# Kernel tuning notes

Hardware: AMD Instinct MI355X
Metric: run time of the kernel (lower is better)

## Reference

```python
import jax, jax.numpy as jnp
import numpy as np

B, T, H, V = 32, 64, 512, 32000


def setup_inputs() -> dict:
    key = jax.random.key(0)
    ks = jax.random.split(key, 8)
    s = 1.0 / np.sqrt(H)
    return {
        "encoder_outputs": jax.random.normal(ks[0], (B, H), dtype=jnp.float32),
        "captions": jax.random.randint(ks[1], (B, T), 0, V),
        "emb": jax.random.normal(ks[2], (V, H), dtype=jnp.float32) * 0.02,
        "W_ih": jax.random.normal(ks[3], (4 * H, 2 * H), dtype=jnp.float32) * s,
        "W_hh": jax.random.normal(ks[4], (4 * H, H), dtype=jnp.float32) * s,
        "b_ih": jnp.zeros((4 * H,), dtype=jnp.float32),
        "b_hh": jnp.zeros((4 * H,), dtype=jnp.float32),
        "W_out": jax.random.normal(ks[5], (V, H), dtype=jnp.float32) * s,
        "b_out": jnp.zeros((V,), dtype=jnp.float32),
    }


def reference(encoder_outputs, captions, emb, W_ih, W_hh, b_ih, b_hh, W_out, b_out):
    Bn, Tn = captions.shape
    Hn = encoder_outputs.shape[-1]
    embeddings = emb[captions]  # (B, T, H)
    # per-step LSTM input: concat(image feature, token embedding) -> (T-1, B, 2H)
    enc = jnp.broadcast_to(encoder_outputs[None], (Tn - 1, Bn, Hn))
    xs = jnp.concatenate([enc, jnp.swapaxes(embeddings[:, : Tn - 1], 0, 1)], axis=-1)
    # precompute input-to-hidden gate contribution outside the scan
    gx = jnp.einsum("tbi,gi->tbg", xs, W_ih) + b_ih  # (T-1, B, 4H)

    h0 = jnp.zeros((Bn, Hn), dtype=encoder_outputs.dtype)
    c0 = jnp.zeros((Bn, Hn), dtype=encoder_outputs.dtype)

    def step(carry, gx_t):
        h, c = carry
        gates = gx_t + h @ W_hh.T + b_hh  # (B, 4H); PyTorch gate order i,f,g,o
        i, f, g, o = jnp.split(gates, 4, axis=-1)
        c = jax.nn.sigmoid(f) * c + jax.nn.sigmoid(i) * jnp.tanh(g)
        h = jax.nn.sigmoid(o) * jnp.tanh(c)
        logit = h @ W_out.T + b_out  # (B, V)
        return (h, c), logit

    _, logits = jax.lax.scan(step, (h0, c0), gx)  # (T-1, B, V)
    logits = jnp.swapaxes(logits, 0, 1)  # (B, T-1, V)
    caption_probs = jnp.max(logits, axis=-1)
    pred_captions = jnp.argmax(logits, axis=-1)
    return logits, caption_probs, pred_captions
```

## Files before the change

kernel.cpp:

```cpp
#include <hip/hip_runtime.h>
#include <hip/hip_bf16.h>
#include <cstdio>


typedef _Float16 half8_t __attribute__((ext_vector_type(8)));
typedef float f32x4_t __attribute__((ext_vector_type(4)));
typedef _Float16 half2_t __attribute__((ext_vector_type(2)));

#define H 512
#define BATCH 32
#define TSTEPS 63
#define G4 2048
#define V 32000

__global__ void k_gxe(const float* __restrict__ enc, const float* __restrict__ W_ih,
                      const float* __restrict__ b_ih, const float* __restrict__ b_hh,
                      float* __restrict__ gxe) {
  __shared__ float sW[16 * 512];
  __shared__ float sP[16 * 8 * 32];
  int tid = threadIdx.x;
  int jg = blockIdx.x;
  #pragma unroll
  for (int rep = 0; rep < 8; ++rep) {
    int q = tid + rep * 256;
    int row = q >> 7, c4 = q & 127;
    float4 v = *(const float4*)(W_ih + (size_t)(jg * 16 + row) * 1024 + c4 * 4);
    *(float4*)(sW + row * 512 + c4 * 4) = v;
  }
  int b = tid & 31, kg = tid >> 5;
  float hreg[64];
  const float* ep = enc + b * 512 + kg * 64;
  #pragma unroll
  for (int i = 0; i < 64; ++i) hreg[i] = ep[i];
  __syncthreads();
  #pragma unroll
  for (int r = 0; r < 16; ++r) {
    float acc = 0.f;
    const float* wp = sW + r * 512 + kg * 64;
    #pragma unroll
    for (int i = 0; i < 64; ++i) acc += hreg[i] * wp[i];
    sP[(r * 8 + kg) * 32 + b] = acc;
  }
  __syncthreads();
  for (int o = tid; o < 512; o += 256) {
    int r = o >> 5, bb = o & 31;
    float s = 0.f;
    #pragma unroll
    for (int k2 = 0; k2 < 8; ++k2) s += sP[(r * 8 + k2) * 32 + bb];
    int j = jg * 16 + r;
    gxe[bb * 2048 + j] = s + b_ih[j] + b_hh[j];
  }
}

__global__ void k_f32_to_f16(const float* __restrict__ src, _Float16* __restrict__ dst) {
  size_t i = ((size_t)blockIdx.x * 256 + threadIdx.x) * 8;
  float4 a = *(const float4*)(src + i);
  float4 b = *(const float4*)(src + i + 4);
  half8_t o;
  o[0] = (_Float16)a.x; o[1] = (_Float16)a.y; o[2] = (_Float16)a.z; o[3] = (_Float16)a.w;
  o[4] = (_Float16)b.x; o[5] = (_Float16)b.y; o[6] = (_Float16)b.z; o[7] = (_Float16)b.w;
  *(half8_t*)(dst + i) = o;
}

__global__ void k_gin(const float* __restrict__ emb, const int* __restrict__ caps,
                      const float* __restrict__ W_ih, const float* __restrict__ gxe,
                      float* __restrict__ ginT) {
  __shared__ float sA[64 * 36];
  __shared__ float sB[64 * 36];
  int tid = threadIdx.x;
  int nb = blockIdx.x;
  int mb = blockIdx.y;
  float acc[4][4] = {};
  int tx = tid & 15, ty = tid >> 4;
  for (int k0 = 0; k0 < 512; k0 += 32) {
    __syncthreads();
    #pragma unroll
    for (int rep = 0; rep < 2; ++rep) {
      int q = tid + rep * 256;
      int row = q >> 3, c4 = q & 7;
      int m = mb * 64 + row;
      int t = m >> 5, b = m & 31;
      if (t > 62) t = 62;
      int tok = caps[b * 64 + t];
      float4 v = *(const float4*)(emb + (size_t)tok * 512 + k0 + c4 * 4);
      *(float4*)(sA + row * 36 + c4 * 4) = v;
      int n = nb * 64 + row;
      float4 w = *(const float4*)(W_ih + (size_t)n * 1024 + 512 + k0 + c4 * 4);
      *(float4*)(sB + row * 36 + c4 * 4) = w;
    }
    __syncthreads();
    #pragma unroll
    for (int kk = 0; kk < 32; ++kk) {
      float a4[4], b4[4];
      #pragma unroll
      for (int i = 0; i < 4; ++i) a4[i] = sA[(ty * 4 + i) * 36 + kk];
      #pragma unroll
      for (int j = 0; j < 4; ++j) b4[j] = sB[(tx * 4 + j) * 36 + kk];
      #pragma unroll
      for (int i = 0; i < 4; ++i)
        #pragma unroll
        for (int j = 0; j < 4; ++j) acc[i][j] += a4[i] * b4[j];
    }
  }
  #pragma unroll
  for (int i = 0; i < 4; ++i) {
    int m = mb * 64 + ty * 4 + i;
    if (m >= 2016) break;
    int t = m >> 5, b = m & 31;
    #pragma unroll
    for (int j = 0; j < 4; ++j) {
      int n = nb * 64 + tx * 4 + j;
      ginT[(size_t)t * 65536 + (size_t)n * 32 + b] = acc[i][j] + gxe[b * 2048 + n];
    }
  }
}

__global__ void k_step(const float* __restrict__ hT_prev, const float* __restrict__ W_hh,
                       const float* __restrict__ ginT_t, float* __restrict__ cT,
                       float* __restrict__ hT_out, _Float16* __restrict__ hf16_t) {
  __shared__ float sW[8 * 512];
  __shared__ float sP[8 * 8 * 32];
  __shared__ float sG[8 * 32];
  int tid = threadIdx.x, kb = blockIdx.x;
  int kbase = kb * 2;
  #pragma unroll
  for (int rep = 0; rep < 4; ++rep) {
    int q = tid + rep * 256;
    int row = q >> 7, c4 = q & 127;
    int j = (row >> 1) * 512 + kbase + (row & 1);
    float4 v = *(const float4*)(W_hh + (size_t)j * 512 + c4 * 4);
    *(float4*)(sW + row * 512 + c4 * 4) = v;
  }
  int b = tid & 31, kg = tid >> 5;
  float hreg[64];
  const float* hp = hT_prev + kg * 64 * 32 + b;
  #pragma unroll
  for (int i = 0; i < 64; ++i) hreg[i] = hp[i * 32];
  __syncthreads();
  #pragma unroll
  for (int r = 0; r < 8; ++r) {
    float acc = 0.f;
    const float* wp = sW + r * 512 + kg * 64;
    #pragma unroll
    for (int i = 0; i < 64; ++i) acc += hreg[i] * wp[i];
    sP[(r * 8 + kg) * 32 + b] = acc;
  }
  __syncthreads();
  {
    int r = tid >> 5;
    float s = 0.f;
    #pragma unroll
    for (int k2 = 0; k2 < 8; ++k2) s += sP[(r * 8 + k2) * 32 + b];
    int j = (r >> 1) * 512 + kbase + (r & 1);
    sG[r * 32 + b] = s + ginT_t[(size_t)j * 32 + b];
  }
  __syncthreads();
  if (tid < 64) {
    int kl = tid >> 5;
    int k = kbase + kl;
    float gi = sG[(0 * 2 + kl) * 32 + b];
    float gf = sG[(1 * 2 + kl) * 32 + b];
    float gg = sG[(2 * 2 + kl) * 32 + b];
    float go = sG[(3 * 2 + kl) * 32 + b];
    float si = 1.f / (1.f + expf(-gi));
    float sf = 1.f / (1.f + expf(-gf));
    float so = 1.f / (1.f + expf(-go));
    float tg = tanhf(gg);
    float c = sf * cT[k * 32 + b] + si * tg;
    float h = so * tanhf(c);
    cT[k * 32 + b] = c;
    hT_out[k * 32 + b] = h;
    hf16_t[(size_t)b * 512 + k] = (_Float16)h;
  }
}

#define ALD 40
__global__ void k_logits(const _Float16* __restrict__ A,
                         const _Float16* __restrict__ B,
                         const float* __restrict__ bias,
                         float* __restrict__ out,
                         float* __restrict__ tmv) {
  __shared__ _Float16 sA[128 * ALD];
  __shared__ _Float16 sB[128 * ALD];
  __shared__ float redv[128 * 2];
  int tid = threadIdx.x;
  int nb = blockIdx.x;
  int mb = blockIdx.y;
  int lane = tid & 63, wave = tid >> 6;
  int wm = wave >> 1, wn = wave & 1;
  const int m0 = mb * 128, n0 = nb * 128;
  f32x4_t acc[4][4] = {};
  int rA = lane & 15, q8 = lane >> 4;
  for (int k0 = 0; k0 < 512; k0 += 32) {
    __syncthreads();
    #pragma unroll
    for (int rep = 0; rep < 2; ++rep) {
      int q = tid + rep * 256;
      int row = q >> 2, seg = q & 3;
      *(half8_t*)(sA + row * ALD + seg * 8) =
          *(const half8_t*)(A + (size_t)(m0 + row) * 512 + k0 + seg * 8);
      *(half8_t*)(sB + row * ALD + seg * 8) =
          *(const half8_t*)(B + (size_t)(n0 + row) * 512 + k0 + seg * 8);
    }
    __syncthreads();
    half8_t afr[4], bfr[4];
    #pragma unroll
    for (int i = 0; i < 4; ++i) {
      afr[i] = *(const half8_t*)(sA + (wm * 64 + i * 16 + rA) * ALD + q8 * 8);
      bfr[i] = *(const half8_t*)(sB + (wn * 64 + i * 16 + rA) * ALD + q8 * 8);
    }
    #pragma unroll
    for (int i = 0; i < 4; ++i)
      #pragma unroll
      for (int j = 0; j < 4; ++j)
        acc[i][j] = __builtin_amdgcn_mfma_f32_16x16x32_f16(afr[i], bfr[j], acc[i][j], 0, 0, 0);
  }
  #pragma unroll
  for (int i = 0; i < 4; ++i) {
    #pragma unroll
    for (int p = 0; p < 4; ++p) {
      int m_loc = wm * 64 + i * 16 + q8 * 4 + p;
      int m = m0 + m_loc;
      float vmax = -3.4e38f;
      float vs[4];
      #pragma unroll
      for (int j = 0; j < 4; ++j) {
        int n_loc = wn * 64 + j * 16 + rA;
        float v = acc[i][j][p] + bias[n0 + n_loc];
        vs[j] = v;
        vmax = fmaxf(vmax, v);
      }
      if (m < 2016) {
        int t = m >> 5, bb = m & 31;
        float* orow = out + (size_t)(bb * 63 + t) * 32000 + n0;
        #pragma unroll
        for (int j = 0; j < 4; ++j) orow[wn * 64 + j * 16 + rA] = vs[j];
      }
      #pragma unroll
      for (int o = 1; o < 16; o <<= 1) vmax = fmaxf(vmax, __shfl_xor(vmax, o));
      if (rA == 0) redv[m_loc * 2 + wn] = vmax;
    }
  }
  __syncthreads();
  if (tid < 128) {
    int m = m0 + tid;
    if (m < 2016) {
      float bv = fmaxf(redv[tid * 2], redv[tid * 2 + 1]);
      tmv[(size_t)m * 256 + nb] = bv;
    }
  }
}

__global__ void k_final(const float* __restrict__ tmv, const float* __restrict__ HallT,
                        const float* __restrict__ Wout, const float* __restrict__ bias,
                        const float* __restrict__ logits,
                        float* __restrict__ probs, float* __restrict__ preds) {
  int m = blockIdx.x;
  int t = m >> 5, b = m & 31;
  int lane = threadIdx.x;
  float mx = -3.4e38f;
  for (int nb = lane; nb < 250; nb += 64) mx = fmaxf(mx, tmv[(size_t)m * 256 + nb]);
  #pragma unroll
  for (int o = 1; o < 64; o <<= 1) mx = fmaxf(mx, __shfl_xor(mx, o));
  const float* hrow = HallT + (size_t)t * 16384 + b;
  float hl[8];
  float s2 = 0.f;
  #pragma unroll
  for (int i = 0; i < 8; ++i) {
    float hv = hrow[(lane * 8 + i) * 32];
    hl[i] = hv;
    s2 += hv * hv;
  }
  #pragma unroll
  for (int o = 1; o < 64; o <<= 1) s2 += __shfl_xor(s2, o);
  float marg = 0.0016f * sqrtf(s2) + 3e-4f;
  float thr = mx - 2.f * marg;
  float bestv = -3.4e38f;
  int besti = 0x7fffffff;
  const float* lrow = logits + (size_t)(b * 63 + t) * 32000;
  for (int nb = 0; nb < 250; ++nb) {
    if (tmv[(size_t)m * 256 + nb] < thr) continue;
    #pragma unroll
    for (int rep = 0; rep < 2; ++rep) {
      int n = nb * 128 + rep * 64 + lane;
      float av = lrow[n];
      unsigned long long mask = __ballot(av >= thr);
      while (mask) {
        int ln = __ffsll((unsigned long long)mask) - 1;
        mask &= mask - 1;
        int nn = __shfl(n, ln);
        const float* wr = Wout + (size_t)nn * 512;
        float p = 0.f;
        #pragma unroll
        for (int i = 0; i < 8; ++i) p += hl[i] * wr[lane * 8 + i];
        #pragma unroll
        for (int o = 1; o < 64; o <<= 1) p += __shfl_xor(p, o);
        p += bias[nn];
        if (p > bestv || (p == bestv && nn < besti)) { bestv = p; besti = nn; }
      }
    }
  }
  if (lane == 0) {
    probs[b * 63 + t] = bestv;
    preds[b * 63 + t] = (float)besti;
  }
}

extern "C" void kernel_launch(void* const* d_in, const int* in_sizes, int n_in,
                              void* d_out, int out_size, void* d_ws, size_t ws_size,
                              hipStream_t stream) {
  const float* enc   = (const float*)d_in[0];
  const int*   caps  = (const int*)d_in[1];
  const float* emb   = (const float*)d_in[2];
  const float* W_ih  = (const float*)d_in[3];
  const float* W_hh  = (const float*)d_in[4];
  const float* b_ih  = (const float*)d_in[5];
  const float* b_hh  = (const float*)d_in[6];
  const float* W_out = (const float*)d_in[7];
  const float* b_out = (const float*)d_in[8];
  float* out = (float*)d_out;

  char* ws = (char*)d_ws;
  const size_t off_gin  = 0;
  const size_t off_gxe  = 16777216;
  const size_t off_hall = off_gxe + 262144;
  const size_t off_hf16 = off_hall + 4194304;
  const size_t off_c    = off_hf16 + 2097152;
  const size_t off_hz   = off_c + 65536;
  const size_t off_tmv  = off_hz + 65536;
  const size_t off_wf16 = off_tmv + 2097152;
  const size_t need     = off_wf16 + 32768000;
  if (ws_size < need) {
    fprintf(stderr, "kernel_launch: ws_size %zu < needed %zu\n", ws_size, need);
    return;
  }
  float*     ginT  = (float*)(ws + off_gin);
  float*     gxe   = (float*)(ws + off_gxe);
  float*     HallT = (float*)(ws + off_hall);
  _Float16*  Hf16  = (_Float16*)(ws + off_hf16);
  float*     cT    = (float*)(ws + off_c);
  float*     hzero = (float*)(ws + off_hz);
  float*     tmv   = (float*)(ws + off_tmv);
  _Float16*  Wf16  = (_Float16*)(ws + off_wf16);

  hipMemsetAsync(ws + off_c, 0, 131072, stream);

  k_gxe<<<128, 256, 0, stream>>>(enc, W_ih, b_ih, b_hh, gxe);
  k_f32_to_f16<<<8000, 256, 0, stream>>>(W_out, Wf16);
  k_gin<<<dim3(32, 32), 256, 0, stream>>>(emb, caps, W_ih, gxe, ginT);

  for (int t = 0; t < 63; ++t) {
    const float* hprev = (t == 0) ? hzero : (HallT + (size_t)(t - 1) * 16384);
    k_step<<<256, 256, 0, stream>>>(hprev, W_hh, ginT + (size_t)t * 65536, cT,
                                    HallT + (size_t)t * 16384, Hf16 + (size_t)t * 16384);
  }

  k_logits<<<dim3(250, 16), 256, 0, stream>>>(Hf16, Wf16, b_out, out, tmv);

  float* probs = out + (size_t)2016 * 32000;
  float* preds = probs + 2016;
  k_final<<<2016, 64, 0, stream>>>(tmv, HallT, W_out, b_out, out, probs, preds);
}
```

Baseline: 1.068 ms.

## Replace FP32 input-gate GEMM with split-FP16 MFMA GEMM

Replaces the scalar FP32 tiled GEMM that computes embedding-to-gate contributions with an MFMA-based kernel. Operands are pre-split into fp16 hi/lo pairs and combined with three MFMAs to keep close to FP32 accuracy. The fp16 buffers temporarily reuse the W_out fp16 workspace before that conversion runs. This adds two prep kernels and extra memory traffic in exchange for matrix-core throughput. The input GEMM is a small share of the total, which is dominated by the 63 sequential step launches and the logits GEMM.

```diff
diff --git a/kernel.cpp b/kernel.cpp
--- a/kernel.cpp
+++ b/kernel.cpp
@@ -4,8 +4,8 @@
 
 
 typedef _Float16 half8_t __attribute__((ext_vector_type(8)));
+typedef _Float16 half4_t __attribute__((ext_vector_type(4)));
 typedef float f32x4_t __attribute__((ext_vector_type(4)));
-typedef _Float16 half2_t __attribute__((ext_vector_type(2)));
 
 #define H 512
 #define BATCH 32
@@ -62,55 +62,114 @@
   *(half8_t*)(dst + i) = o;
 }
 
-__global__ void k_gin(const float* __restrict__ emb, const int* __restrict__ caps,
-                      const float* __restrict__ W_ih, const float* __restrict__ gxe,
-                      float* __restrict__ ginT) {
-  __shared__ float sA[64 * 36];
-  __shared__ float sB[64 * 36];
+__global__ void k_prep_w(const float* __restrict__ W_ih, _Float16* __restrict__ hi,
+                         _Float16* __restrict__ lo) {
+  size_t idx = ((size_t)blockIdx.x * 256 + threadIdx.x) * 4;
+  int row = (int)(idx >> 9), col = (int)(idx & 511);
+  float4 v = *(const float4*)(W_ih + (size_t)row * 1024 + 512 + col);
+  half4_t vh, vl;
+  vh[0] = (_Float16)v.x; vl[0] = (_Float16)(v.x - (float)vh[0]);
+  vh[1] = (_Float16)v.y; vl[1] = (_Float16)(v.y - (float)vh[1]);
+  vh[2] = (_Float16)v.z; vl[2] = (_Float16)(v.z - (float)vh[2]);
+  vh[3] = (_Float16)v.w; vl[3] = (_Float16)(v.w - (float)vh[3]);
+  *(half4_t*)(hi + idx) = vh;
+  *(half4_t*)(lo + idx) = vl;
+}
+
+__global__ void k_prep_x(const float* __restrict__ emb, const int* __restrict__ caps,
+                         _Float16* __restrict__ hi, _Float16* __restrict__ lo) {
+  int m = blockIdx.x * 4 + (threadIdx.x >> 6);
+  int lane = threadIdx.x & 63;
+  size_t o = (size_t)m * 512 + lane * 8;
+  half8_t vh = {}, vl = {};
+  if (m < 2016) {
+    int t = m >> 5, b = m & 31;
+    int tok = caps[b * 64 + t];
+    const float* src = emb + (size_t)tok * 512 + lane * 8;
+    float4 a = *(const float4*)(src);
+    float4 c = *(const float4*)(src + 4);
+    float vs[8] = {a.x, a.y, a.z, a.w, c.x, c.y, c.z, c.w};
+    #pragma unroll
+    for (int i = 0; i < 8; ++i) {
+      vh[i] = (_Float16)vs[i];
+      vl[i] = (_Float16)(vs[i] - (float)vh[i]);
+    }
+  }
+  *(half8_t*)(hi + o) = vh;
+  *(half8_t*)(lo + o) = vl;
+}
+
+#define ALD 40
+__global__ void k_gin_mfma(const _Float16* __restrict__ Whi, const _Float16* __restrict__ Wlo,
+                           const _Float16* __restrict__ Xhi, const _Float16* __restrict__ Xlo,
+                           const float* __restrict__ gxe, float* __restrict__ ginT) {
+  __shared__ _Float16 sAhi[128 * ALD];
+  __shared__ _Float16 sAlo[128 * ALD];
+  __shared__ _Float16 sBhi[128 * ALD];
+  __shared__ _Float16 sBlo[128 * ALD];
+  __shared__ float sGxe[32 * 132];
   int tid = threadIdx.x;
   int nb = blockIdx.x;
   int mb = blockIdx.y;
-  float acc[4][4] = {};
-  int tx = tid & 15, ty = tid >> 4;
+  int lane = tid & 63, wave = tid >> 6;
+  int wm = wave >> 1, wn = wave & 1;
+  const int m0 = mb * 128, n0 = nb * 128;
+  int rA = lane & 15, q8 = lane >> 4;
+  for (int q = tid; q < 1024; q += 256) {
+    int b = q >> 5, c4 = q & 31;
+    float4 v = *(const float4*)(gxe + (size_t)b * 2048 + m0 + c4 * 4);
+    float* d = sGxe + b * 132 + c4 * 4;
+    d[0] = v.x; d[1] = v.y; d[2] = v.z; d[3] = v.w;
+  }
+  f32x4_t acc[4][4] = {};
   for (int k0 = 0; k0 < 512; k0 += 32) {
     __syncthreads();
     #pragma unroll
-    for (int rep = 0; rep < 2; ++rep) {
-      int q = tid + rep * 256;
-      int row = q >> 3, c4 = q & 7;
-      int m = mb * 64 + row;
-      int t = m >> 5, b = m & 31;
-      if (t > 62) t = 62;
-      int tok = caps[b * 64 + t];
-      float4 v = *(const float4*)(emb + (size_t)tok * 512 + k0 + c4 * 4);
-      *(float4*)(sA + row * 36 + c4 * 4) = v;
-      int n = nb * 64 + row;
-      float4 w = *(const float4*)(W_ih + (size_t)n * 1024 + 512 + k0 + c4 * 4);
-      *(float4*)(sB + row * 36 + c4 * 4) = w;
+    for (int rep = 0; rep < 8; ++rep) {
+      int q = rep * 256 + tid;
+      int buf = q >> 9, r = q & 511, row = r >> 2, seg = r & 3;
+      const _Float16* gsrc;
+      _Float16* ldst;
+      if (buf == 0)      { gsrc = Whi + (size_t)(m0 + row) * 512; ldst = sAhi; }
+      else if (buf == 1) { gsrc = Wlo + (size_t)(m0 + row) * 512; ldst = sAlo; }
+      else if (buf == 2) { gsrc = Xhi + (size_t)(n0 + row) * 512; ldst = sBhi; }
+      else               { gsrc = Xlo + (size_t)(n0 + row) * 512; ldst = sBlo; }
+      *(half8_t*)(ldst + row * ALD + seg * 8) = *(const half8_t*)(gsrc + k0 + seg * 8);
     }
     __syncthreads();
-    #pragma unroll
-    for (int kk = 0; kk < 32; ++kk) {
-      float a4[4], b4[4];
+    half8_t ah[4], al[4], bh[4], bl[4];
+    #pragma unroll
+    for (int i = 0; i < 4; ++i) {
+      int ra = (wm * 64 + i * 16 + rA) * ALD + q8 * 8;
+      ah[i] = *(const half8_t*)(sAhi + ra);
+      al[i] = *(const half8_t*)(sAlo + ra);
+      int rb = (wn * 64 + i * 16 + rA) * ALD + q8 * 8;
+      bh[i] = *(const half8_t*)(sBhi + rb);
+      bl[i] = *(const half8_t*)(sBlo + rb);
+    }
+    #pragma unroll
+    for (int i = 0; i < 4; ++i)
       #pragma unroll
-      for (int i = 0; i < 4; ++i) a4[i] = sA[(ty * 4 + i) * 36 + kk];
+      for (int j = 0; j < 4; ++j) {
+        acc[i][j] = __builtin_amdgcn_mfma_f32_16x16x32_f16(ah[i], bh[j], acc[i][j], 0, 0, 0);
+        acc[i][j] = __builtin_amdgcn_mfma_f32_16x16x32_f16(ah[i], bl[j], acc[i][j], 0, 0, 0);
+        acc[i][j] = __builtin_amdgcn_mfma_f32_16x16x32_f16(al[i], bh[j], acc[i][j], 0, 0, 0);
+      }
+  }
+  #pragma unroll
+  for (int i = 0; i < 4; ++i) {
+    #pragma unroll
+    for (int p = 0; p < 4; ++p) {
+      int jg_loc = wm * 64 + i * 16 + q8 * 4 + p;
+      int jg = m0 + jg_loc;
       #pragma unroll
-      for (int j = 0; j < 4; ++j) b4[j] = sB[(tx * 4 + j) * 36 + kk];
-      #pragma unroll
-      for (int i = 0; i < 4; ++i)
-        #pragma unroll
-        for (int j = 0; j < 4; ++j) acc[i][j] += a4[i] * b4[j];
-    }
-  }
-  #pragma unroll
-  for (int i = 0; i < 4; ++i) {
-    int m = mb * 64 + ty * 4 + i;
-    if (m >= 2016) break;
-    int t = m >> 5, b = m & 31;
-    #pragma unroll
-    for (int j = 0; j < 4; ++j) {
-      int n = nb * 64 + tx * 4 + j;
-      ginT[(size_t)t * 65536 + (size_t)n * 32 + b] = acc[i][j] + gxe[b * 2048 + n];
+      for (int j = 0; j < 4; ++j) {
+        int m = n0 + wn * 64 + j * 16 + rA;
+        if (m < 2016) {
+          int t = m >> 5, b = m & 31;
+          ginT[(size_t)t * 65536 + (size_t)jg * 32 + b] = acc[i][j][p] + sGxe[b * 132 + jg_loc];
+        }
+      }
     }
   }
 }
@@ -174,7 +233,6 @@
   }
 }
 
-#define ALD 40
 __global__ void k_logits(const _Float16* __restrict__ A,
                          const _Float16* __restrict__ B,
                          const float* __restrict__ bias,
@@ -342,12 +400,18 @@
   float*     hzero = (float*)(ws + off_hz);
   float*     tmv   = (float*)(ws + off_tmv);
   _Float16*  Wf16  = (_Float16*)(ws + off_wf16);
+  _Float16*  Xhi = Wf16;
+  _Float16*  Xlo = Xhi + 2048 * 512;
+  _Float16*  Whi = Xlo + 2048 * 512;
+  _Float16*  Wlo = Whi + 2048 * 512;
 
   hipMemsetAsync(ws + off_c, 0, 131072, stream);
 
   k_gxe<<<128, 256, 0, stream>>>(enc, W_ih, b_ih, b_hh, gxe);
+  k_prep_w<<<1024, 256, 0, stream>>>(W_ih, Whi, Wlo);
+  k_prep_x<<<512, 256, 0, stream>>>(emb, caps, Xhi, Xlo);
+  k_gin_mfma<<<dim3(16, 16), 256, 0, stream>>>(Whi, Wlo, Xhi, Xlo, gxe, ginT);
   k_f32_to_f16<<<8000, 256, 0, stream>>>(W_out, Wf16);
-  k_gin<<<dim3(32, 32), 256, 0, stream>>>(emb, caps, W_ih, gxe, ginT);
 
   for (int t = 0; t < 63; ++t) {
     const float* hprev = (t == 0) ? hzero : (HallT + (size_t)(t - 1) * 16384);
```

Result: faster. 917.6 us (-14.1%).
